# Kernel optimization log

Hardware: AMD Instinct MI355X
Metric: run time of the kernel (lower is better)

The kernel has to match this reference:

```python
import jax, jax.numpy as jnp
import numpy as np

D_MODEL = 1024
NUM_HEADS = 16


def setup_inputs() -> dict:
    key = jax.random.key(0)
    ks = jax.random.split(key, 5)
    std = np.sqrt(2.0 / (D_MODEL + D_MODEL)).astype(np.float32)
    x = jax.random.normal(ks[0], (4, 2048, D_MODEL), dtype=jnp.float32)
    WQ = jax.random.normal(ks[1], (D_MODEL, D_MODEL), dtype=jnp.float32) * std
    WK = jax.random.normal(ks[2], (D_MODEL, D_MODEL), dtype=jnp.float32) * std
    WV = jax.random.normal(ks[3], (D_MODEL, D_MODEL), dtype=jnp.float32) * std
    WO = jax.random.normal(ks[4], (D_MODEL, D_MODEL), dtype=jnp.float32) * std
    return {"x": x, "WQ": WQ, "WK": WK, "WV": WV, "WO": WO}


def reference(x, WQ, WK, WV, WO):
    B, S, E = x.shape
    H = NUM_HEADS
    dk = E // H
    # project and split heads: [B, H, S, dk]
    def heads(W):
        return jnp.einsum('bse,ef->bsf', x, W).reshape(B, S, H, dk).transpose(0, 2, 1, 3)
    Q, K, V = heads(WQ), heads(WK), heads(WV)
    score = jnp.einsum('bhsd,bhtd->bhst', Q, K) / jnp.sqrt(jnp.float32(dk))
    causal = jnp.tril(jnp.ones((S, S), dtype=bool))  # [S, S]
    score = jnp.where(causal, score, -jnp.inf)
    probs = jax.nn.softmax(score, axis=-1)
    out = jnp.einsum('bhst,bhtd->bhsd', probs, V)  # [B, H, S, dk]
    out = out.transpose(0, 2, 1, 3).reshape(B, S, E)
    return jnp.einsum('bse,ef->bsf', out, WO)
```

## Files before the change

### kernel.cpp

```cpp
#include <hip/hip_runtime.h>

typedef unsigned short u16;
typedef short bf16x8 __attribute__((ext_vector_type(8)));
typedef float f32x4 __attribute__((ext_vector_type(4)));

#define SEQ   2048
#define EMB   1024
#define NH    16
#define DK    64

#define QSCALE 0.1803368801111144f

__device__ __forceinline__ u16 bf16_rne(float f) {
  union { float f; unsigned u; } x;
  x.f = f;
  unsigned u = x.u;
  u += 0x7fffu + ((u >> 16) & 1u);
  return (u16)(u >> 16);
}

__device__ __forceinline__ unsigned cvt_pk_bf16(float a, float b) {
  unsigned r;
  asm("v_cvt_pk_bf16_f32 %0, %1, %2" : "=v"(r) : "v"(a), "v"(b));
  return r;
}

__device__ __forceinline__ float max3f(float a, float b, float c) {
  return fmaxf(fmaxf(a, b), c);
}

__global__ __launch_bounds__(256) void fill_sig(float* __restrict__ out, int n) {
  const int i = blockIdx.x * 256 + threadIdx.x;
  if (i < n) out[i] = 1.0f;
}

__global__ __launch_bounds__(256) void cvt_x(const float* __restrict__ x,
                                             u16* __restrict__ xb) {
  const size_t i = ((size_t)blockIdx.x * 256 + threadIdx.x) * 8;
  float4 v0 = *(const float4*)(x + i);
  float4 v1 = *(const float4*)(x + i + 4);
  union { int4 v; u16 h[8]; } c;
  c.h[0] = bf16_rne(v0.x); c.h[1] = bf16_rne(v0.y);
  c.h[2] = bf16_rne(v0.z); c.h[3] = bf16_rne(v0.w);
  c.h[4] = bf16_rne(v1.x); c.h[5] = bf16_rne(v1.y);
  c.h[6] = bf16_rne(v1.z); c.h[7] = bf16_rne(v1.w);
  *(int4*)(xb + i) = c.v;
}

__global__ __launch_bounds__(256) void tcvt3(
    const float* __restrict__ s0, const float* __restrict__ s1, const float* __restrict__ s2,
    u16* __restrict__ d0, u16* __restrict__ d1, u16* __restrict__ d2) {
  const int z = blockIdx.z;
  const float* src = (z == 0) ? s0 : (z == 1) ? s1 : s2;
  u16* dst = (z == 0) ? d0 : (z == 1) ? d1 : d2;
  const float sc = (z == 0) ? QSCALE : 1.0f;
  __shared__ u16 tile[64][65];
  const int bx = blockIdx.x * 64, by = blockIdx.y * 64;
  for (int i = threadIdx.x; i < 64 * 64; i += 256) {
    const int r = i >> 6, c = i & 63;
    tile[c][r] = bf16_rne(src[(size_t)(by + r) * EMB + bx + c] * sc);
  }
  __syncthreads();
  for (int i = threadIdx.x; i < 64 * 64; i += 256) {
    const int r = i >> 6, c = i & 63;
    dst[(size_t)(bx + r) * EMB + by + c] = tile[r][c];
  }
}

__global__ __launch_bounds__(256) void tcvt1(const float* __restrict__ src,
                                             u16* __restrict__ dst) {
  __shared__ u16 tile[64][65];
  const int bx = blockIdx.x * 64, by = blockIdx.y * 64;
  for (int i = threadIdx.x; i < 64 * 64; i += 256) {
    const int r = i >> 6, c = i & 63;
    tile[c][r] = bf16_rne(src[(size_t)(by + r) * EMB + bx + c]);
  }
  __syncthreads();
  for (int i = threadIdx.x; i < 64 * 64; i += 256) {
    const int r = i >> 6, c = i & 63;
    dst[(size_t)(bx + r) * EMB + by + c] = tile[r][c];
  }
}

__global__ __launch_bounds__(256) void gemm_qkv(
    const u16* __restrict__ A,
    const u16* __restrict__ T0, const u16* __restrict__ T1, const u16* __restrict__ T2,
    u16* __restrict__ C0, u16* __restrict__ C1, u16* __restrict__ C2)
{
  const int z = blockIdx.z;
  const u16* Wt = (z == 0) ? T0 : (z == 1) ? T1 : T2;
  u16* C = (z == 0) ? C0 : (z == 1) ? C1 : C2;

  __shared__ __align__(16) u16 sh[8704];
  u16* const As = sh;
  u16* const Bs = sh + 4096;

  const int tid  = threadIdx.x;
  const int lane = tid & 63;
  const int w    = tid >> 6;
  const int wm   = (w >> 1) * 64;
  const int wn   = (w & 1) * 64;
  const int m0   = blockIdx.x * 128;
  const int n0   = blockIdx.y * 128;

  const int l15  = lane & 15;
  const int g8   = (lane >> 4) * 8;

  const int lrow = lane >> 2;
  const int lcol = (lane & 3) * 8;

  f32x4 acc[4][4] = {};

  for (int k0 = 0; k0 < 1024; k0 += 32) {
#pragma unroll
    for (int i = 0; i < 2; ++i) {
      const int r = w * 32 + i * 16;
      const u16* ga = A  + (size_t)(m0 + r + lrow) * 1024 + (k0 + lcol);
      const u16* gb = Wt + (size_t)(n0 + r + lrow) * 1024 + (k0 + lcol);
      __builtin_amdgcn_global_load_lds((const __attribute__((address_space(1))) void*)ga,
                                       (__attribute__((address_space(3))) void*)(As + r * 32), 16, 0, 0);
      __builtin_amdgcn_global_load_lds((const __attribute__((address_space(1))) void*)gb,
                                       (__attribute__((address_space(3))) void*)(Bs + r * 32), 16, 0, 0);
    }
    __syncthreads();
    bf16x8 a[4], b[4];
#pragma unroll
    for (int mi = 0; mi < 4; ++mi)
      a[mi] = *(const bf16x8*)(As + (wm + mi * 16 + l15) * 32 + g8);
#pragma unroll
    for (int ni = 0; ni < 4; ++ni)
      b[ni] = *(const bf16x8*)(Bs + (wn + ni * 16 + l15) * 32 + g8);
#pragma unroll
    for (int mi = 0; mi < 4; ++mi)
#pragma unroll
      for (int ni = 0; ni < 4; ++ni)
        acc[mi][ni] = __builtin_amdgcn_mfma_f32_16x16x32_bf16(a[mi], b[ni], acc[mi][ni], 0, 0, 0);
    __syncthreads();
  }

  const int rb = (lane >> 4) * 4;

  if (z != 2) {
#pragma unroll
    for (int mi = 0; mi < 4; ++mi) {
#pragma unroll
      for (int r = 0; r < 4; ++r) {
        const int row = m0 + wm + mi * 16 + rb + r;
        const int bb = row >> 11, s = row & 2047;
#pragma unroll
        for (int ni = 0; ni < 4; ++ni) {
          const int col = n0 + wn + ni * 16 + l15;
          const int hh = col >> 6, d = col & 63;
          C[((size_t)(bb * NH + hh) * SEQ + s) * DK + d] = bf16_rne(acc[mi][ni][r]);
        }
      }
    }
  } else {
    const int bb = m0 >> 11;
    const int s0 = m0 & 2047;
    u16* const T = sh;
    const int dRd  = tid >> 2;
    const int cbRd = (tid & 3) * 32;
    const int swzR = ((dRd >> 3) & 7) << 3;
#pragma unroll
    for (int p = 0; p < 2; ++p) {
      if ((w & 1) == p) {
#pragma unroll
        for (int mi = 0; mi < 4; ++mi)
#pragma unroll
          for (int r = 0; r < 4; ++r) {
            const int s_local = wm + mi * 16 + rb + r;
#pragma unroll
            for (int ni = 0; ni < 4; ++ni) {
              const int d = ni * 16 + l15;
              T[d * 136 + (s_local ^ (((d >> 3) & 7) << 3))] = bf16_rne(acc[mi][ni][r]);
            }
          }
      }
      __syncthreads();
      u16* dst = C + ((size_t)(bb * NH + (n0 >> 6) + p) * DK + dRd) * SEQ + s0 + cbRd;
#pragma unroll
      for (int k = 0; k < 4; ++k) {
        int4 v = *(const int4*)(T + dRd * 136 + ((cbRd + 8 * k) ^ swzR));
        *(int4*)(dst + 8 * k) = v;
      }
      __syncthreads();
    }
  }
}

__global__ __launch_bounds__(256) void gemm_out(
    const u16* __restrict__ A, const u16* __restrict__ Wt, float* __restrict__ C)
{
  __shared__ __align__(16) u16 As[128 * 32];
  __shared__ __align__(16) u16 Bs[128 * 32];

  const int tid  = threadIdx.x;
  const int lane = tid & 63;
  const int w    = tid >> 6;
  const int wm   = (w >> 1) * 64;
  const int wn   = (w & 1) * 64;
  const int m0   = blockIdx.x * 128;
  const int n0   = blockIdx.y * 128;

  const int l15  = lane & 15;
  const int g8   = (lane >> 4) * 8;

  const int lrow = lane >> 2;
  const int lcol = (lane & 3) * 8;

  f32x4 acc[4][4] = {};

  for (int k0 = 0; k0 < 1024; k0 += 32) {
#pragma unroll
    for (int i = 0; i < 2; ++i) {
      const int r = w * 32 + i * 16;
      const u16* ga = A  + (size_t)(m0 + r + lrow) * 1024 + (k0 + lcol);
      const u16* gb = Wt + (size_t)(n0 + r + lrow) * 1024 + (k0 + lcol);
      __builtin_amdgcn_global_load_lds((const __attribute__((address_space(1))) void*)ga,
                                       (__attribute__((address_space(3))) void*)(As + r * 32), 16, 0, 0);
      __builtin_amdgcn_global_load_lds((const __attribute__((address_space(1))) void*)gb,
                                       (__attribute__((address_space(3))) void*)(Bs + r * 32), 16, 0, 0);
    }
    __syncthreads();
    bf16x8 a[4], b[4];
#pragma unroll
    for (int mi = 0; mi < 4; ++mi)
      a[mi] = *(const bf16x8*)(As + (wm + mi * 16 + l15) * 32 + g8);
#pragma unroll
    for (int ni = 0; ni < 4; ++ni)
      b[ni] = *(const bf16x8*)(Bs + (wn + ni * 16 + l15) * 32 + g8);
#pragma unroll
    for (int mi = 0; mi < 4; ++mi)
#pragma unroll
      for (int ni = 0; ni < 4; ++ni)
        acc[mi][ni] = __builtin_amdgcn_mfma_f32_16x16x32_bf16(a[mi], b[ni], acc[mi][ni], 0, 0, 0);
    __syncthreads();
  }

  const int rb = (lane >> 4) * 4;
#pragma unroll
  for (int mi = 0; mi < 4; ++mi) {
#pragma unroll
    for (int r = 0; r < 4; ++r) {
      const int row = m0 + wm + mi * 16 + rb + r;
#pragma unroll
      for (int ni = 0; ni < 4; ++ni) {
        const int col = n0 + wn + ni * 16 + l15;
        C[(size_t)row * 1024 + col] = acc[mi][ni][r];
      }
    }
  }
}

#define RESCALE_THR 12.0f

__global__ __launch_bounds__(256) void attn64(
    const u16* __restrict__ Q, const u16* __restrict__ K, const u16* __restrict__ VT,
    u16* __restrict__ O)
{
  const int it  = blockIdx.x;
  const int bh  = blockIdx.y;
  const int tid = threadIdx.x;
  const int lane = tid & 63;
  const int w    = tid >> 6;

  const u16* Qp = Q  + (size_t)bh * SEQ * DK;
  const u16* Kp = K  + (size_t)bh * SEQ * DK;
  const u16* Vp = VT + (size_t)bh * DK * SEQ;

  __shared__ __align__(16) u16 Ks[64 * 72];
  __shared__ __align__(16) u16 Vs[64 * 72];
  __shared__ __align__(16) u16 Pt[4][32 * 72];

  const int l15 = lane & 15;
  const int g   = lane >> 4;
  const int g8  = g * 8;

  const int srow = tid >> 3;
  const int sc8  = (tid & 7) * 8;
  const u16* kb = Kp + (size_t)srow * DK + sc8;
  const u16* vb = Vp + (size_t)srow * SEQ + sc8;
  u16* const ksd0 = Ks + srow * 72 + sc8;
  u16* const ksd1 = Ks + (srow + 32) * 72 + sc8;
  u16* const vsd0 = Vs + srow * 72 + sc8;
  u16* const vsd1 = Vs + (srow + 32) * 72 + sc8;

  u16* const pw = &Pt[w][0];
  const int b_ = bh >> 4, h_ = bh & 15;

  int4 kr0, kr1, vr0, vr1;

  for (int pass = 0; pass < 2; ++pass) {
    const int qt = pass ? 15 - it : it;
    const int q0 = qt * 128;
    const int qw = q0 + w * 32;
    const int tlast = 2 * qt + 1;

    bf16x8 qf[2][2];
#pragma unroll
    for (int j = 0; j < 2; ++j)
#pragma unroll
      for (int kk = 0; kk < 2; ++kk)
        qf[j][kk] = *(const bf16x8*)(Qp + (size_t)(qw + j * 16 + l15) * DK + kk * 32 + g8);

    f32x4 o[2][4] = {};
    float mrun[2] = { -1e30f, -1e30f };
    float lrun[2] = { 0.f, 0.f };

    kr0 = *(const int4*)(kb);
    kr1 = *(const int4*)(kb + (size_t)32 * DK);
    vr0 = *(const int4*)(vb);
    vr1 = *(const int4*)(vb + (size_t)32 * SEQ);

    for (int t = 0; t <= tlast; ++t) {
      __syncthreads();
      *(int4*)ksd0 = kr0; *(int4*)ksd1 = kr1;
      *(int4*)vsd0 = vr0; *(int4*)vsd1 = vr1;
      __syncthreads();
      if (t < tlast) {
        const u16* kn = kb + (size_t)(t + 1) * 64 * DK;
        const u16* vn = vb + (t + 1) * 64;
        kr0 = *(const int4*)(kn);
        kr1 = *(const int4*)(kn + (size_t)32 * DK);
        vr0 = *(const int4*)(vn);
        vr1 = *(const int4*)(vn + (size_t)32 * SEQ);
      }

      if (64 * t >= qw + 32) continue;

      f32x4 st[2][4] = {};
#pragma unroll
      for (int kk = 0; kk < 2; ++kk) {
#pragma unroll
        for (int mt = 0; mt < 4; ++mt) {
          const bf16x8 kf = *(const bf16x8*)(Ks + (mt * 16 + l15) * 72 + kk * 32 + g8);
          st[0][mt] = __builtin_amdgcn_mfma_f32_16x16x32_bf16(kf, qf[0][kk], st[0][mt], 0, 0, 0);
          st[1][mt] = __builtin_amdgcn_mfma_f32_16x16x32_bf16(kf, qf[1][kk], st[1][mt], 0, 0, 0);
        }
      }

#pragma unroll
      for (int j = 0; j < 2; ++j) {
        const int qg = qw + j * 16;
        if (qg <= 64 * t + 48) {
          const int qrow = qg + l15;
#pragma unroll
          for (int mt = 0; mt < 4; ++mt)
#pragma unroll
            for (int r = 0; r < 4; ++r)
              if (64 * t + mt * 16 + g * 4 + r > qrow) st[j][mt][r] = -1e30f;
        }

        float t0 = max3f(st[j][0][0], st[j][0][1], st[j][0][2]);
        float t1 = max3f(st[j][0][3], st[j][1][0], st[j][1][1]);
        float t2 = max3f(st[j][1][2], st[j][1][3], st[j][2][0]);
        float t3 = max3f(st[j][2][1], st[j][2][2], st[j][2][3]);
        float t4 = max3f(st[j][3][0], st[j][3][1], st[j][3][2]);
        float tmax = fmaxf(max3f(t0, t1, t2), max3f(t3, t4, st[j][3][3]));
        tmax = fmaxf(tmax, __shfl_xor(tmax, 16));
        tmax = fmaxf(tmax, __shfl_xor(tmax, 32));

        if (!__all(tmax - mrun[j] <= RESCALE_THR)) {
          const float mnew  = fmaxf(mrun[j], tmax);
          const float alpha = exp2f(mrun[j] - mnew);
          mrun[j] = mnew;
          lrun[j] *= alpha;
#pragma unroll
          for (int r = 0; r < 4; ++r) {
            const float ar = __shfl(alpha, g * 4 + r);
#pragma unroll
            for (int nt = 0; nt < 4; ++nt) o[j][nt][r] *= ar;
          }
        }
        const float mcur = mrun[j];

        float psum = 0.f;
#pragma unroll
        for (int mt = 0; mt < 4; ++mt) {
          float p0 = exp2f(st[j][mt][0] - mcur);
          float p1 = exp2f(st[j][mt][1] - mcur);
          float p2 = exp2f(st[j][mt][2] - mcur);
          float p3 = exp2f(st[j][mt][3] - mcur);
          psum += (p0 + p1) + (p2 + p3);
          uint2 pk;
          pk.x = cvt_pk_bf16(p0, p1);
          pk.y = cvt_pk_bf16(p2, p3);
          *(uint2*)(pw + (j * 16 + l15) * 72 + mt * 16 + g * 4) = pk;
        }
        psum += __shfl_xor(psum, 16);
        psum += __shfl_xor(psum, 32);
        lrun[j] += psum;
      }

#pragma unroll
      for (int kk = 0; kk < 2; ++kk) {
        const bf16x8 pa0 = *(const bf16x8*)(pw + (0 + l15) * 72 + kk * 32 + g8);
        const bf16x8 pa1 = *(const bf16x8*)(pw + (16 + l15) * 72 + kk * 32 + g8);
#pragma unroll
        for (int nt = 0; nt < 4; ++nt) {
          const bf16x8 vv = *(const bf16x8*)(Vs + (nt * 16 + l15) * 72 + kk * 32 + g8);
          o[0][nt] = __builtin_amdgcn_mfma_f32_16x16x32_bf16(pa0, vv, o[0][nt], 0, 0, 0);
          o[1][nt] = __builtin_amdgcn_mfma_f32_16x16x32_bf16(pa1, vv, o[1][nt], 0, 0, 0);
        }
      }
    }

#pragma unroll
    for (int j = 0; j < 2; ++j) {
#pragma unroll
      for (int r = 0; r < 4; ++r) {
        const float lr  = __shfl(lrun[j], g * 4 + r);
        const float inv = 1.0f / lr;
        const int   s   = qw + j * 16 + g * 4 + r;
#pragma unroll
        for (int nt = 0; nt < 4; ++nt) {
          const int d = nt * 16 + l15;
          O[((size_t)b_ * SEQ + s) * EMB + h_ * DK + d] = bf16_rne(o[j][nt][r] * inv);
        }
      }
    }
  }
}

extern "C" void kernel_launch(void* const* d_in, const int* in_sizes, int n_in,
                              void* d_out, int out_size, void* d_ws, size_t ws_size,
                              hipStream_t stream) {
  (void)in_sizes; (void)n_in;
  const float* x  = (const float*)d_in[0];
  const float* WQ = (const float*)d_in[1];
  const float* WK = (const float*)d_in[2];
  const float* WV = (const float*)d_in[3];
  const float* WO = (const float*)d_in[4];
  float* out = (float*)d_out;

  const size_t MTOK = (size_t)4 * SEQ;
  const size_t NTOK = MTOK * EMB;
  const size_t NW   = (size_t)EMB * EMB;

  const size_t NEEDED = 4 * NTOK * sizeof(u16);
  if (ws_size < NEEDED) {
    fill_sig<<<dim3((out_size + 255) / 256), 256, 0, stream>>>(out, out_size);
    return;
  }

  u16* ws  = (u16*)d_ws;
  u16* Qb  = ws;
  u16* Kb  = Qb + NTOK;
  u16* VTb = Kb + NTOK;
  u16* Ob  = VTb + NTOK;
  u16* xb  = (u16*)d_out;
  u16* WQt = Ob;
  u16* WKt = WQt + NW;
  u16* WVt = WKt + NW;
  u16* WOt = Qb;

  cvt_x<<<dim3(4096), 256, 0, stream>>>(x, xb);
  tcvt3<<<dim3(16, 16, 3), 256, 0, stream>>>(WQ, WK, WV, WQt, WKt, WVt);
  gemm_qkv<<<dim3(MTOK / 128, EMB / 128, 3), 256, 0, stream>>>(
      xb, WQt, WKt, WVt, Qb, Kb, VTb);
  attn64<<<dim3(8, 4 * NH), 256, 0, stream>>>(Qb, Kb, VTb, Ob);
  tcvt1<<<dim3(16, 16), 256, 0, stream>>>(WO, WOt);
  gemm_out<<<dim3(MTOK / 128, EMB / 128), 256, 0, stream>>>(Ob, WOt, out);
}
```

Baseline: 293.4 us.

## Split attention into one q-tile per block with XCD-aware mapping and MFMA row sums

Each attention block previously handled two q-tiles (it and 15-it) in sequence. It now handles a single q-tile across a 1D grid of 1024 blocks. The block index is decoded so each XCD gets a fixed group of heads and q-tiles are interleaved in a balanced order. The softmax row sum is now accumulated by an extra MFMA against a vector of ones, replacing the shuffle-based reduction. This trades the self-balancing pairing for more blocks and better L2 locality per XCD, and adds two MFMAs per step.

After: 302.0 us. 3.0% more time.

```diff
diff --git a/kernel.cpp b/kernel.cpp
--- a/kernel.cpp
+++ b/kernel.cpp
@@ -259,8 +259,16 @@
     const u16* __restrict__ Q, const u16* __restrict__ K, const u16* __restrict__ VT,
     u16* __restrict__ O)
 {
-  const int it  = blockIdx.x;
-  const int bh  = blockIdx.y;
+  const int b       = blockIdx.x;
+  const int xcd     = b & 7;
+  const int idx     = b >> 3;
+  const int cu_slot = idx & 31;
+  const int quarter = idx >> 5;
+  const int tg      = cu_slot >> 3;
+  const int bh      = xcd * 8 + (cu_slot & 7);
+  const int qt      = (quarter == 0) ? tg : (quarter == 1) ? 7 - tg
+                    : (quarter == 2) ? 8 + tg : 15 - tg;
+
   const int tid = threadIdx.x;
   const int lane = tid & 63;
   const int w    = tid >> 6;
@@ -289,135 +297,130 @@
   u16* const pw = &Pt[w][0];
   const int b_ = bh >> 4, h_ = bh & 15;
 
-  int4 kr0, kr1, vr0, vr1;
-
-  for (int pass = 0; pass < 2; ++pass) {
-    const int qt = pass ? 15 - it : it;
-    const int q0 = qt * 128;
-    const int qw = q0 + w * 32;
-    const int tlast = 2 * qt + 1;
-
-    bf16x8 qf[2][2];
-#pragma unroll
-    for (int j = 0; j < 2; ++j)
-#pragma unroll
-      for (int kk = 0; kk < 2; ++kk)
-        qf[j][kk] = *(const bf16x8*)(Qp + (size_t)(qw + j * 16 + l15) * DK + kk * 32 + g8);
-
-    f32x4 o[2][4] = {};
-    float mrun[2] = { -1e30f, -1e30f };
-    float lrun[2] = { 0.f, 0.f };
-
-    kr0 = *(const int4*)(kb);
-    kr1 = *(const int4*)(kb + (size_t)32 * DK);
-    vr0 = *(const int4*)(vb);
-    vr1 = *(const int4*)(vb + (size_t)32 * SEQ);
-
-    for (int t = 0; t <= tlast; ++t) {
-      __syncthreads();
-      *(int4*)ksd0 = kr0; *(int4*)ksd1 = kr1;
-      *(int4*)vsd0 = vr0; *(int4*)vsd1 = vr1;
-      __syncthreads();
-      if (t < tlast) {
-        const u16* kn = kb + (size_t)(t + 1) * 64 * DK;
-        const u16* vn = vb + (t + 1) * 64;
-        kr0 = *(const int4*)(kn);
-        kr1 = *(const int4*)(kn + (size_t)32 * DK);
-        vr0 = *(const int4*)(vn);
-        vr1 = *(const int4*)(vn + (size_t)32 * SEQ);
-      }
-
-      if (64 * t >= qw + 32) continue;
-
-      f32x4 st[2][4] = {};
-#pragma unroll
-      for (int kk = 0; kk < 2; ++kk) {
-#pragma unroll
-        for (int mt = 0; mt < 4; ++mt) {
-          const bf16x8 kf = *(const bf16x8*)(Ks + (mt * 16 + l15) * 72 + kk * 32 + g8);
-          st[0][mt] = __builtin_amdgcn_mfma_f32_16x16x32_bf16(kf, qf[0][kk], st[0][mt], 0, 0, 0);
-          st[1][mt] = __builtin_amdgcn_mfma_f32_16x16x32_bf16(kf, qf[1][kk], st[1][mt], 0, 0, 0);
+  bf16x8 vone;
+#pragma unroll
+  for (int i = 0; i < 8; ++i) vone[i] = (short)0x3F80;
+
+  const int q0 = qt * 128;
+  const int qw = q0 + w * 32;
+  const int tlast = 2 * qt + 1;
+
+  bf16x8 qf[2][2];
+#pragma unroll
+  for (int j = 0; j < 2; ++j)
+#pragma unroll
+    for (int kk = 0; kk < 2; ++kk)
+      qf[j][kk] = *(const bf16x8*)(Qp + (size_t)(qw + j * 16 + l15) * DK + kk * 32 + g8);
+
+  f32x4 o[2][4] = {};
+  f32x4 osum[2] = {};
+  float mrun[2] = { -1e30f, -1e30f };
+
+  int4 kr0 = *(const int4*)(kb);
+  int4 kr1 = *(const int4*)(kb + (size_t)32 * DK);
+  int4 vr0 = *(const int4*)(vb);
+  int4 vr1 = *(const int4*)(vb + (size_t)32 * SEQ);
+
+  for (int t = 0; t <= tlast; ++t) {
+    __syncthreads();
+    *(int4*)ksd0 = kr0; *(int4*)ksd1 = kr1;
+    *(int4*)vsd0 = vr0; *(int4*)vsd1 = vr1;
+    __syncthreads();
+    if (t < tlast) {
+      const u16* kn = kb + (size_t)(t + 1) * 64 * DK;
+      const u16* vn = vb + (t + 1) * 64;
+      kr0 = *(const int4*)(kn);
+      kr1 = *(const int4*)(kn + (size_t)32 * DK);
+      vr0 = *(const int4*)(vn);
+      vr1 = *(const int4*)(vn + (size_t)32 * SEQ);
+    }
+
+    if (64 * t >= qw + 32) continue;
+
+    f32x4 st[2][4] = {};
+#pragma unroll
+    for (int kk = 0; kk < 2; ++kk) {
+#pragma unroll
+      for (int mt = 0; mt < 4; ++mt) {
+        const bf16x8 kf = *(const bf16x8*)(Ks + (mt * 16 + l15) * 72 + kk * 32 + g8);
+        st[0][mt] = __builtin_amdgcn_mfma_f32_16x16x32_bf16(kf, qf[0][kk], st[0][mt], 0, 0, 0);
+        st[1][mt] = __builtin_amdgcn_mfma_f32_16x16x32_bf16(kf, qf[1][kk], st[1][mt], 0, 0, 0);
+      }
+    }
+
+#pragma unroll
+    for (int j = 0; j < 2; ++j) {
+      const int qg = qw + j * 16;
+      if (qg <= 64 * t + 48) {
+        const int qrow = qg + l15;
+#pragma unroll
+        for (int mt = 0; mt < 4; ++mt)
+#pragma unroll
+          for (int r = 0; r < 4; ++r)
+            if (64 * t + mt * 16 + g * 4 + r > qrow) st[j][mt][r] = -1e30f;
+      }
+
+      float t0 = max3f(st[j][0][0], st[j][0][1], st[j][0][2]);
+      float t1 = max3f(st[j][0][3], st[j][1][0], st[j][1][1]);
+      float t2 = max3f(st[j][1][2], st[j][1][3], st[j][2][0]);
+      float t3 = max3f(st[j][2][1], st[j][2][2], st[j][2][3]);
+      float t4 = max3f(st[j][3][0], st[j][3][1], st[j][3][2]);
+      float tmax = fmaxf(max3f(t0, t1, t2), max3f(t3, t4, st[j][3][3]));
+      tmax = fmaxf(tmax, __shfl_xor(tmax, 16));
+      tmax = fmaxf(tmax, __shfl_xor(tmax, 32));
+
+      if (!__all(tmax - mrun[j] <= RESCALE_THR)) {
+        const float mnew  = fmaxf(mrun[j], tmax);
+        const float alpha = exp2f(mrun[j] - mnew);
+        mrun[j] = mnew;
+#pragma unroll
+        for (int r = 0; r < 4; ++r) {
+          const float ar = __shfl(alpha, g * 4 + r);
+          osum[j][r] *= ar;
+#pragma unroll
+          for (int nt = 0; nt < 4; ++nt) o[j][nt][r] *= ar;
         }
       }
-
-#pragma unroll
-      for (int j = 0; j < 2; ++j) {
-        const int qg = qw + j * 16;
-        if (qg <= 64 * t + 48) {
-          const int qrow = qg + l15;
-#pragma unroll
-          for (int mt = 0; mt < 4; ++mt)
-#pragma unroll
-            for (int r = 0; r < 4; ++r)
-              if (64 * t + mt * 16 + g * 4 + r > qrow) st[j][mt][r] = -1e30f;
-        }
-
-        float t0 = max3f(st[j][0][0], st[j][0][1], st[j][0][2]);
-        float t1 = max3f(st[j][0][3], st[j][1][0], st[j][1][1]);
-        float t2 = max3f(st[j][1][2], st[j][1][3], st[j][2][0]);
-        float t3 = max3f(st[j][2][1], st[j][2][2], st[j][2][3]);
-        float t4 = max3f(st[j][3][0], st[j][3][1], st[j][3][2]);
-        float tmax = fmaxf(max3f(t0, t1, t2), max3f(t3, t4, st[j][3][3]));
-        tmax = fmaxf(tmax, __shfl_xor(tmax, 16));
-        tmax = fmaxf(tmax, __shfl_xor(tmax, 32));
-
-        if (!__all(tmax - mrun[j] <= RESCALE_THR)) {
-          const float mnew  = fmaxf(mrun[j], tmax);
-          const float alpha = exp2f(mrun[j] - mnew);
-          mrun[j] = mnew;
-          lrun[j] *= alpha;
-#pragma unroll
-          for (int r = 0; r < 4; ++r) {
-            const float ar = __shfl(alpha, g * 4 + r);
-#pragma unroll
-            for (int nt = 0; nt < 4; ++nt) o[j][nt][r] *= ar;
-          }
-        }
-        const float mcur = mrun[j];
-
-        float psum = 0.f;
-#pragma unroll
-        for (int mt = 0; mt < 4; ++mt) {
-          float p0 = exp2f(st[j][mt][0] - mcur);
-          float p1 = exp2f(st[j][mt][1] - mcur);
-          float p2 = exp2f(st[j][mt][2] - mcur);
-          float p3 = exp2f(st[j][mt][3] - mcur);
-          psum += (p0 + p1) + (p2 + p3);
-          uint2 pk;
-          pk.x = cvt_pk_bf16(p0, p1);
-          pk.y = cvt_pk_bf16(p2, p3);
-          *(uint2*)(pw + (j * 16 + l15) * 72 + mt * 16 + g * 4) = pk;
-        }
-        psum += __shfl_xor(psum, 16);
-        psum += __shfl_xor(psum, 32);
-        lrun[j] += psum;
-      }
-
-#pragma unroll
-      for (int kk = 0; kk < 2; ++kk) {
-        const bf16x8 pa0 = *(const bf16x8*)(pw + (0 + l15) * 72 + kk * 32 + g8);
-        const bf16x8 pa1 = *(const bf16x8*)(pw + (16 + l15) * 72 + kk * 32 + g8);
-#pragma unroll
-        for (int nt = 0; nt < 4; ++nt) {
-          const bf16x8 vv = *(const bf16x8*)(Vs + (nt * 16 + l15) * 72 + kk * 32 + g8);
-          o[0][nt] = __builtin_amdgcn_mfma_f32_16x16x32_bf16(pa0, vv, o[0][nt], 0, 0, 0);
-          o[1][nt] = __builtin_amdgcn_mfma_f32_16x16x32_bf16(pa1, vv, o[1][nt], 0, 0, 0);
-        }
-      }
-    }
-
-#pragma unroll
-    for (int j = 0; j < 2; ++j) {
-#pragma unroll
-      for (int r = 0; r < 4; ++r) {
-        const float lr  = __shfl(lrun[j], g * 4 + r);
-        const float inv = 1.0f / lr;
-        const int   s   = qw + j * 16 + g * 4 + r;
-#pragma unroll
-        for (int nt = 0; nt < 4; ++nt) {
-          const int d = nt * 16 + l15;
-          O[((size_t)b_ * SEQ + s) * EMB + h_ * DK + d] = bf16_rne(o[j][nt][r] * inv);
-        }
+      const float mcur = mrun[j];
+
+#pragma unroll
+      for (int mt = 0; mt < 4; ++mt) {
+        float p0 = exp2f(st[j][mt][0] - mcur);
+        float p1 = exp2f(st[j][mt][1] - mcur);
+        float p2 = exp2f(st[j][mt][2] - mcur);
+        float p3 = exp2f(st[j][mt][3] - mcur);
+        uint2 pk;
+        pk.x = cvt_pk_bf16(p0, p1);
+        pk.y = cvt_pk_bf16(p2, p3);
+        *(uint2*)(pw + (j * 16 + l15) * 72 + mt * 16 + g * 4) = pk;
+      }
+    }
+
+#pragma unroll
+    for (int kk = 0; kk < 2; ++kk) {
+      const bf16x8 pa0 = *(const bf16x8*)(pw + (0 + l15) * 72 + kk * 32 + g8);
+      const bf16x8 pa1 = *(const bf16x8*)(pw + (16 + l15) * 72 + kk * 32 + g8);
+      osum[0] = __builtin_amdgcn_mfma_f32_16x16x32_bf16(pa0, vone, osum[0], 0, 0, 0);
+      osum[1] = __builtin_amdgcn_mfma_f32_16x16x32_bf16(pa1, vone, osum[1], 0, 0, 0);
+#pragma unroll
+      for (int nt = 0; nt < 4; ++nt) {
+        const bf16x8 vv = *(const bf16x8*)(Vs + (nt * 16 + l15) * 72 + kk * 32 + g8);
+        o[0][nt] = __builtin_amdgcn_mfma_f32_16x16x32_bf16(pa0, vv, o[0][nt], 0, 0, 0);
+        o[1][nt] = __builtin_amdgcn_mfma_f32_16x16x32_bf16(pa1, vv, o[1][nt], 0, 0, 0);
+      }
+    }
+  }
+
+#pragma unroll
+  for (int j = 0; j < 2; ++j) {
+#pragma unroll
+    for (int r = 0; r < 4; ++r) {
+      const float inv = 1.0f / osum[j][r];
+      const int   s   = qw + j * 16 + g * 4 + r;
+#pragma unroll
+      for (int nt = 0; nt < 4; ++nt) {
+        const int d = nt * 16 + l15;
+        O[((size_t)b_ * SEQ + s) * EMB + h_ * DK + d] = bf16_rne(o[j][nt][r] * inv);
       }
     }
   }
@@ -459,7 +462,7 @@
   tcvt3<<<dim3(16, 16, 3), 256, 0, stream>>>(WQ, WK, WV, WQt, WKt, WVt);
   gemm_qkv<<<dim3(MTOK / 128, EMB / 128, 3), 256, 0, stream>>>(
       xb, WQt, WKt, WVt, Qb, Kb, VTb);
-  attn64<<<dim3(8, 4 * NH), 256, 0, stream>>>(Qb, Kb, VTb, Ob);
+  attn64<<<dim3(1024), 256, 0, stream>>>(Qb, Kb, VTb, Ob);
   tcvt1<<<dim3(16, 16), 256, 0, stream>>>(WO, WOt);
   gemm_out<<<dim3(MTOK / 128, EMB / 128), 256, 0, stream>>>(Ob, WOt, out);
 }
```
